# Kernel optimization log

Hardware: AMD Instinct MI355X
Metric: run time of the kernel (lower is better)

Reference implementation:

```python
import jax, jax.numpy as jnp
import numpy as np

N_NODES = 50000
N_EDGES = 1600000
IN_DIM = 128
HEADS = 4
HEAD_DIM = 32  # out_dim // heads
N_REL = 3
NEG_SLOPE = 0.2


def setup_inputs() -> dict:
    key = jax.random.key(0)
    ks = jax.random.split(key, 8)
    x = jax.random.normal(ks[0], (N_NODES, IN_DIM), dtype=jnp.float32)
    edge_index = jax.random.randint(ks[1], (2, N_EDGES), 0, N_NODES, dtype=jnp.int64)
    edge_type = jax.random.randint(ks[2], (N_EDGES,), 0, N_REL, dtype=jnp.int64)
    # per-relation GATConv params (PyG layout: lin weight, att_src, att_dst, bias)
    s = 1.0 / np.sqrt(IN_DIM)
    W = jax.random.normal(ks[3], (N_REL, IN_DIM, HEADS * HEAD_DIM), dtype=jnp.float32) * s
    att_src = jax.random.normal(ks[4], (N_REL, HEADS, HEAD_DIM), dtype=jnp.float32) * s
    att_dst = jax.random.normal(ks[5], (N_REL, HEADS, HEAD_DIM), dtype=jnp.float32) * s
    bias = jnp.zeros((N_REL, HEADS * HEAD_DIM), dtype=jnp.float32)
    rel_w = jnp.ones((N_REL,), dtype=jnp.float32)  # relation_weights param
    return {"x": x, "W": W, "att_src": att_src, "att_dst": att_dst,
            "bias": bias, "rel_w": rel_w,
            "edge_index": edge_index, "edge_type": edge_type}


def reference(x, W, att_src, att_dst, bias, rel_w, edge_index, edge_type):
    N = x.shape[0]
    NEG = jnp.float32(-1e9)
    # self loops (GATConv add_self_loops=True) appended; present in every relation
    self_idx = jnp.arange(N, dtype=edge_index.dtype)
    src = jnp.concatenate([edge_index[0], self_idx])  # [E+N]
    dst = jnp.concatenate([edge_index[1], self_idx])  # [E+N]
    weights = jax.nn.softmax(rel_w)
    out = jnp.zeros((N, HEADS * HEAD_DIM), dtype=x.dtype)
    for r in range(N_REL):
        h = (x @ W[r]).reshape(N, HEADS, HEAD_DIM)  # [N,H,C]
        a_s = jnp.einsum('nhc,hc->nh', h, att_src[r])
        a_d = jnp.einsum('nhc,hc->nh', h, att_dst[r])
        score = jax.nn.leaky_relu(a_s[src] + a_d[dst], NEG_SLOPE)  # [E+N,H]
        mask = jnp.concatenate([edge_type == r, jnp.ones((N,), dtype=bool)])
        score = jnp.where(mask[:, None], score, NEG)  # mask out other relations
        # segment softmax over incoming edges per destination node
        smax = jax.ops.segment_max(score, dst, num_segments=N)  # finite: self-loops
        ex = jnp.exp(score - smax[dst])
        denom = jax.ops.segment_sum(ex, dst, num_segments=N)
        alpha = ex / denom[dst]  # [E+N,H]
        msg = alpha[:, :, None] * h[src]  # [E+N,H,C]
        rel_out = jax.ops.segment_sum(msg, dst, num_segments=N).reshape(N, HEADS * HEAD_DIM)
        out = out + weights[r] * (rel_out + bias[r])
    return out
```

## Files before the change

kernel.cpp:

```cpp
#include <hip/hip_runtime.h>
#include <hip/hip_bf16.h>
#include <hip/hip_fp16.h>
#include <math.h>

#define IN_DIM 128
#define OUT_DIM 128
#define HEADS 4
#define HEAD_DIM 32
#define NREL 3
#define NEG_SLOPE 0.2f

#define CHUNK 4096
#define BUCK_SHIFT 7
#define DPB 128
#define KPB 384
#define CAPE 6144
#define CAPS (CAPE + 3*DPB)

typedef __attribute__((ext_vector_type(8))) short short8;
typedef __attribute__((ext_vector_type(4))) float f32x4;
typedef unsigned short u16;

static __device__ __forceinline__ float leaky(float x){ return fmaxf(x, NEG_SLOPE*x); }
static __device__ __forceinline__ unsigned bf16rn(float x){
  unsigned b = __float_as_uint(x);
  b += 0x7FFF + ((b>>16)&1u);
  return b>>16;
}
static __device__ __forceinline__ unsigned h2pack(float a, float b){
  union { __half h[2]; unsigned u; } p;
  p.h[0] = __float2half_rn(a); p.h[1] = __float2half_rn(b);
  return p.u;
}

__global__ void k_wprep(const float* __restrict__ W, const float* __restrict__ att_s,
                        const float* __restrict__ att_d, const float* __restrict__ rw,
                        const float* __restrict__ bias, u16* __restrict__ WTall,
                        float* __restrict__ smw, float* __restrict__ biasMix){
  const int r = blockIdx.x;
  const int t = threadIdx.x;
  const float* Wr = W + (size_t)r*IN_DIM*OUT_DIM;
  u16* WT = WTall + (size_t)r*144*128;
  for (int i=t; i<128*128; i+=256){
    int k = i>>7, col = i&127;
    WT[col*128 + k] = (u16)bf16rn(Wr[i]);
  }
  if (t < 128){
    int k = t;
    for (int h=0; h<4; h++){
      float ss=0.f, sd=0.f;
      for (int c=0; c<32; c++){
        float w = Wr[k*128 + h*32 + c];
        ss = fmaf(w, att_s[(r*4+h)*32+c], ss);
        sd = fmaf(w, att_d[(r*4+h)*32+c], sd);
      }
      WT[(128+h)*128 + k] = (u16)bf16rn(ss);
      WT[(132+h)*128 + k] = (u16)bf16rn(sd);
    }
  }
  for (int i=t; i<8*128; i+=256) WT[136*128 + i] = 0;
  if (r == 0){
    float m = fmaxf(rw[0], fmaxf(rw[1], rw[2]));
    float e0=__expf(rw[0]-m), e1=__expf(rw[1]-m), e2=__expf(rw[2]-m);
    float inv = 1.f/(e0+e1+e2);
    if (t < 3) smw[t] = (t==0?e0:(t==1?e1:e2))*inv;
    if (t < 128)
      biasMix[t] = inv*(e0*bias[t] + e1*bias[OUT_DIM+t] + e2*bias[2*OUT_DIM+t]);
  }
}

__global__ __launch_bounds__(256) void k_gemmhist(
    const float* __restrict__ x, const u16* __restrict__ WTall,
    unsigned* __restrict__ hq, float* __restrict__ as_, float* __restrict__ ad_,
    const int* __restrict__ ei, int* __restrict__ histG,
    int N, int E, int NCHUNK, int NBUCK){
  __shared__ int h[512];
  const int t = threadIdx.x;

  if (blockIdx.x < (unsigned)NCHUNK){
    const int c = blockIdx.x;
    h[t] = 0; h[t+256] = 0; __syncthreads();
    const int* dstp = ei + E;
    const int base = c*CHUNK;
    #pragma unroll 4
    for (int it=0; it<CHUNK/256; ++it){
      int e = base + it*256 + t;
      if (e < E) atomicAdd(&h[dstp[e]>>BUCK_SHIFT], 1);
    }
    __syncthreads();
    for (int k=t; k<NBUCK; k+=256) histG[k*NCHUNK + c] = h[k];
    return;
  }

  const int w = t >> 6;
  const int l = t & 63;
  const int row0 = (blockIdx.x - NCHUNK)*128 + w*32;
  const int lg = l >> 4;
  const int lc = l & 15;

  short8 afrag[4][2];
  #pragma unroll
  for (int ks=0; ks<4; ks++){
    const int k0 = ks*32 + lg*8;
    #pragma unroll
    for (int rf=0; rf<2; rf++){
      int row = row0 + rf*16 + lc;
      float4 v0, v1;
      if (row < N){
        const float4* xp = (const float4*)(x + (size_t)row*IN_DIM + k0);
        v0 = xp[0]; v1 = xp[1];
      } else { v0 = float4{0.f,0.f,0.f,0.f}; v1 = v0; }
      union { short8 s; unsigned u[4]; } pa;
      pa.u[0] = bf16rn(v0.x) | (bf16rn(v0.y)<<16);
      pa.u[1] = bf16rn(v0.z) | (bf16rn(v0.w)<<16);
      pa.u[2] = bf16rn(v1.x) | (bf16rn(v1.y)<<16);
      pa.u[3] = bf16rn(v1.z) | (bf16rn(v1.w)<<16);
      afrag[ks][rf] = pa.s;
    }
  }

  for (int r=0; r<NREL; r++){
    const u16* WT = WTall + (size_t)r*144*128;
    f32x4 acc[2][9];
    #pragma unroll
    for (int rf=0; rf<2; rf++)
      #pragma unroll
      for (int cf=0; cf<9; cf++) acc[rf][cf] = (f32x4){0.f,0.f,0.f,0.f};

    #pragma unroll
    for (int ks=0; ks<4; ks++){
      const int k0 = ks*32 + lg*8;
      #pragma unroll
      for (int cf=0; cf<9; cf++){
        short8 b = *(const short8*)(WT + (size_t)(cf*16 + lc)*128 + k0);
        #pragma unroll
        for (int rf=0; rf<2; rf++)
          acc[rf][cf] = __builtin_amdgcn_mfma_f32_16x16x32_bf16(afrag[ks][rf], b, acc[rf][cf], 0, 0, 0);
      }
    }

    #pragma unroll
    for (int rf=0; rf<2; rf++){
      #pragma unroll
      for (int j=0; j<4; j++){
        int row = row0 + rf*16 + lg*4 + j;
        bool ok = (row < N);
        size_t nidx = (size_t)r*N + row;
        #pragma unroll
        for (int cf=0; cf<8; cf++){
          float v = acc[rf][cf][j];
          float pv = __shfl_xor(v, 1);
          if (ok && !(l&1))
            hq[nidx*64 + cf*8 + (lc>>1)] = bf16rn(v) | (bf16rn(pv)<<16);
        }
        float av = acc[rf][8][j];
        if (ok && lc < 4)       as_[nidx*4 + lc]     = av;
        else if (ok && lc < 8)  ad_[nidx*4 + (lc-4)] = av;
      }
    }
  }
}

__global__ __launch_bounds__(256) void k_scanSeg(const int* __restrict__ histG,
                        int* __restrict__ chunkOff, int* __restrict__ totalE, int NCHUNK){
  __shared__ int sh[512];
  __shared__ int ps[256];
  const int b = blockIdx.x, t = threadIdx.x;
  sh[t]     = (t     < NCHUNK) ? histG[b*NCHUNK + t]     : 0;
  sh[t+256] = (t+256 < NCHUNK) ? histG[b*NCHUNK + t+256] : 0;
  __syncthreads();
  int e0 = sh[2*t], pair = e0 + sh[2*t+1];
  ps[t] = pair; __syncthreads();
  int x = pair;
  for (int off=1; off<256; off<<=1){
    int y = (t>=off)?ps[t-off]:0; __syncthreads();
    x += y; ps[t] = x; __syncthreads();
  }
  int ex = x - pair;
  if (2*t   < NCHUNK) chunkOff[b*NCHUNK + 2*t]   = ex;
  if (2*t+1 < NCHUNK) chunkOff[b*NCHUNK + 2*t+1] = ex + e0;
  if (t == 255) totalE[b] = x;
}

__global__ __launch_bounds__(256) void k_part(const int* __restrict__ et, const int* __restrict__ ei,
                       const int* __restrict__ chunkOff, unsigned* __restrict__ payload,
                       int E, int NCHUNK, int NBUCK){
  __shared__ int cur[512];
  const int c = blockIdx.x, t = threadIdx.x;
  for (int k=t; k<NBUCK; k+=256) cur[k] = k*CAPE + chunkOff[k*NCHUNK + c];
  __syncthreads();
  const int* dstp = ei + E;
  const int base = c*CHUNK;
  #pragma unroll 4
  for (int it=0; it<CHUNK/256; ++it){
    int e = base + it*256 + t;
    if (e < E){
      int d = dstp[e];
      int s = ei[e];
      int r = et[e];
      int b = d >> BUCK_SHIFT;
      int pos = atomicAdd(&cur[b], 1);
      payload[pos] = (unsigned)((d & (DPB-1)) | (r<<7) | (s<<9));
    }
  }
}

__global__ __launch_bounds__(512) void k_csr(const unsigned* __restrict__ payload,
                     const int* __restrict__ totalE,
                     const float* __restrict__ as_, const float* __restrict__ ad_,
                     const float* __restrict__ smw,
                     int* __restrict__ offs, unsigned* __restrict__ ssrc2,
                     uint2* __restrict__ alpha, float4* __restrict__ ivg,
                     int E, int N, int NCHUNK, int NBUCK){
  __shared__ int cntA[KPB];
  __shared__ int cur[KPB];
  __shared__ float den[KPB*4];
  __shared__ float4 adl[KPB];
  __shared__ int ps[DPB];
  const int b = blockIdx.x, t = threadIdx.x;
  const int bs = b*CAPE;
  const int be = bs + totalE[b];
  const int outbase = b*CAPS;
  const int validD = min(N - b*DPB, DPB);

  for (int k=t; k<KPB; k+=512) cntA[k] = 0;
  for (int k=t; k<KPB*4; k+=512) den[k] = 0.f;
  for (int k=t; k<KPB; k+=512){
    int dl = k/3, r = k - dl*3;
    int d2 = b*DPB + dl;
    adl[k] = (d2 < N) ? ((const float4*)ad_)[(size_t)r*N + d2] : (float4){0,0,0,0};
  }
  __syncthreads();
  for (int i=bs+t; i<be; i+=512){
    unsigned p = payload[i];
    atomicAdd(&cntA[(int)(p&(DPB-1))*NREL + (int)((p>>7)&3u)], 1);
  }
  __syncthreads();
  const int dst = b*DPB + t;
  int c0=0,c1=0,c2=0,sum=0,o0=0,o1=0,o2=0,hs=0;
  if (t < DPB){
    hs = (dst < N) ? 1 : 0;
    c0 = cntA[3*t]   + hs;
    c1 = cntA[3*t+1] + hs;
    c2 = cntA[3*t+2] + hs;
    sum = c0+c1+c2;
    ps[t] = sum;
  }
  __syncthreads();
  int xsc = sum;
  for (int off=1; off<DPB; off<<=1){
    int y = (t < DPB && t >= off) ? ps[t-off] : 0;
    __syncthreads();
    if (t < DPB) { xsc += y; ps[t] = xsc; }
    __syncthreads();
  }
  if (t < DPB){
    int ex = xsc - sum;
    o0 = outbase + ex; o1 = o0 + c0; o2 = o1 + c1;
    offs[b*(KPB+1) + 3*t]   = o0;
    offs[b*(KPB+1) + 3*t+1] = o1;
    offs[b*(KPB+1) + 3*t+2] = o2;
    cur[3*t]   = (o0 - outbase) + hs;
    cur[3*t+1] = (o1 - outbase) + hs;
    cur[3*t+2] = (o2 - outbase) + hs;
  }
  if (t == 0) offs[b*(KPB+1) + KPB] = outbase + (be - bs) + 3*validD;
  __syncthreads();
  for (int i=bs+t; i<be; i+=512){
    unsigned p = payload[i];
    int dl = (int)(p&(DPB-1)), r = (int)((p>>7)&3u), s = (int)(p>>9);
    int lkey = dl*NREL + r;
    int pos = outbase + atomicAdd(&cur[lkey], 1);
    float4 a4 = ((const float4*)as_)[(size_t)r*N + s];
    float4 b4 = adl[lkey];
    float ex0 = __expf(leaky(a4.x+b4.x));
    float ex1 = __expf(leaky(a4.y+b4.y));
    float ex2 = __expf(leaky(a4.z+b4.z));
    float ex3 = __expf(leaky(a4.w+b4.w));
    ssrc2[pos] = (unsigned)(s | (r<<16));
    alpha[pos] = (uint2){ h2pack(ex0,ex1), h2pack(ex2,ex3) };
    atomicAdd(&den[lkey*4+0], ex0); atomicAdd(&den[lkey*4+1], ex1);
    atomicAdd(&den[lkey*4+2], ex2); atomicAdd(&den[lkey*4+3], ex3);
  }
  __syncthreads();
  if (t < DPB && dst < N){
    int starts[3] = {o0, o1, o2};
    #pragma unroll
    for (int r=0; r<NREL; r++){
      int lkey = 3*t + r;
      float4 a4 = ((const float4*)as_)[(size_t)r*N + dst];
      float4 b4 = adl[lkey];
      float s0 = __expf(leaky(a4.x+b4.x));
      float s1 = __expf(leaky(a4.y+b4.y));
      float s2 = __expf(leaky(a4.z+b4.z));
      float s3 = __expf(leaky(a4.w+b4.w));
      float w = smw[r];
      float4 iv;
      iv.x = w/(den[lkey*4+0]+s0);
      iv.y = w/(den[lkey*4+1]+s1);
      iv.z = w/(den[lkey*4+2]+s2);
      iv.w = w/(den[lkey*4+3]+s3);
      ivg[dst*3 + r] = iv;
      int sp = starts[r];
      ssrc2[sp] = (unsigned)(dst | (r<<16));
      alpha[sp] = (uint2){ h2pack(s0,s1), h2pack(s2,s3) };
    }
  }
}

__global__ __launch_bounds__(128) void k_segment(
    const int* __restrict__ offs, const unsigned* __restrict__ ssrc2,
    const uint2* __restrict__ alpha, const unsigned* __restrict__ hq,
    const float4* __restrict__ ivg, const float* __restrict__ biasMix,
    float* __restrict__ out, int N){
  const int wave = threadIdx.x >> 6;
  const int lane = threadIdx.x & 63;
  const int dst  = blockIdx.x*2 + wave;
  if (dst >= N) return;
  const int g  = lane >> 3;
  const int l8 = lane & 7;
  const int h0 = l8 >> 2;

  const int bb = dst >> BUCK_SHIFT;
  const int lk = (dst & (DPB-1))*3;
  const int* ob = offs + (size_t)bb*(KPB+1);
  int beg = __builtin_amdgcn_readfirstlane(ob[lk]);
  int end = __builtin_amdgcn_readfirstlane(ob[lk+3]);

  float4 v0 = ivg[dst*3+0], v1 = ivg[dst*3+1], v2 = ivg[dst*3+2];
  float iA0 = h0 ? v0.y : v0.x, iB0 = h0 ? v0.w : v0.z;
  float iA1 = h0 ? v1.y : v1.x, iB1 = h0 ? v1.w : v1.z;
  float iA2 = h0 ? v2.y : v2.x, iB2 = h0 ? v2.w : v2.z;

  float acc0[8], acc1[8];
  #pragma unroll
  for (int q=0; q<8; q++){ acc0[q]=0.f; acc1[q]=0.f; }

  for (int i0=beg; i0<end; i0+=16){
    int i = i0 + g;
    int j = i0 + 8 + g;
    bool vi = (i < end), vj = (j < end);
    unsigned pk1=0, pk2=0; uint2 av1={0,0}, av2={0,0};
    if (vi){ pk1 = ssrc2[i]; av1 = alpha[i]; }
    if (vj){ pk2 = ssrc2[j]; av2 = alpha[j]; }
    if (vi){
      int s = (int)(pk1 & 0xFFFFu);
      int r = (int)((pk1 >> 16) & 3u);
      float ivA = (r==0)? iA0 : (r==1)? iA1 : iA2;
      float ivB = (r==0)? iB0 : (r==1)? iB1 : iB2;
      union { unsigned u; __half h[2]; } pa, pb;
      pa.u = av1.x; pb.u = av1.y;
      float a0 = __half2float(pa.h[h0]) * ivA;
      float a1 = __half2float(pb.h[h0]) * ivB;
      const uint4* hp = (const uint4*)(hq + ((size_t)r*N + s)*64 + l8*4);
      uint4 u0 = hp[0];
      uint4 u1 = hp[8];
      const unsigned* p0 = (const unsigned*)&u0;
      const unsigned* p1 = (const unsigned*)&u1;
      #pragma unroll
      for (int q=0; q<4; q++){
        acc0[2*q]   = fmaf(a0, __uint_as_float(p0[q]<<16),           acc0[2*q]);
        acc0[2*q+1] = fmaf(a0, __uint_as_float(p0[q] & 0xFFFF0000u), acc0[2*q+1]);
        acc1[2*q]   = fmaf(a1, __uint_as_float(p1[q]<<16),           acc1[2*q]);
        acc1[2*q+1] = fmaf(a1, __uint_as_float(p1[q] & 0xFFFF0000u), acc1[2*q+1]);
      }
    }
    if (vj){
      int s = (int)(pk2 & 0xFFFFu);
      int r = (int)((pk2 >> 16) & 3u);
      float ivA = (r==0)? iA0 : (r==1)? iA1 : iA2;
      float ivB = (r==0)? iB0 : (r==1)? iB1 : iB2;
      union { unsigned u; __half h[2]; } pa, pb;
      pa.u = av2.x; pb.u = av2.y;
      float a0 = __half2float(pa.h[h0]) * ivA;
      float a1 = __half2float(pb.h[h0]) * ivB;
      const uint4* hp = (const uint4*)(hq + ((size_t)r*N + s)*64 + l8*4);
      uint4 u0 = hp[0];
      uint4 u1 = hp[8];
      const unsigned* p0 = (const unsigned*)&u0;
      const unsigned* p1 = (const unsigned*)&u1;
      #pragma unroll
      for (int q=0; q<4; q++){
        acc0[2*q]   = fmaf(a0, __uint_as_float(p0[q]<<16),           acc0[2*q]);
        acc0[2*q+1] = fmaf(a0, __uint_as_float(p0[q] & 0xFFFF0000u), acc0[2*q+1]);
        acc1[2*q]   = fmaf(a1, __uint_as_float(p1[q]<<16),           acc1[2*q]);
        acc1[2*q+1] = fmaf(a1, __uint_as_float(p1[q] & 0xFFFF0000u), acc1[2*q+1]);
      }
    }
  }

  #pragma unroll
  for (int o=8; o<=32; o<<=1){
    #pragma unroll
    for (int q=0; q<8; q++){
      acc0[q] += __shfl_xor(acc0[q], o);
      acc1[q] += __shfl_xor(acc1[q], o);
    }
  }

  if (g == 0){
    const float4* bmA = (const float4*)(biasMix + 8*l8);
    const float4* bmB = (const float4*)(biasMix + 64 + 8*l8);
    float4 x0 = bmA[0], x1 = bmA[1], y0 = bmB[0], y1 = bmB[1];
    float* orow = out + (size_t)dst*OUT_DIM;
    float4 o0 = {acc0[0]+x0.x, acc0[1]+x0.y, acc0[2]+x0.z, acc0[3]+x0.w};
    float4 o1 = {acc0[4]+x1.x, acc0[5]+x1.y, acc0[6]+x1.z, acc0[7]+x1.w};
    float4 o2 = {acc1[0]+y0.x, acc1[1]+y0.y, acc1[2]+y0.z, acc1[3]+y0.w};
    float4 o3 = {acc1[4]+y1.x, acc1[5]+y1.y, acc1[6]+y1.z, acc1[7]+y1.w};
    *(float4*)(orow + 8*l8)          = o0;
    *(float4*)(orow + 8*l8 + 4)      = o1;
    *(float4*)(orow + 64 + 8*l8)     = o2;
    *(float4*)(orow + 64 + 8*l8 + 4) = o3;
  }
}

extern "C" void kernel_launch(void* const* d_in, const int* in_sizes, int n_in,
                              void* d_out, int out_size, void* d_ws, size_t ws_size,
                              hipStream_t stream) {
  const float* x     = (const float*)d_in[0];
  const float* W     = (const float*)d_in[1];
  const float* att_s = (const float*)d_in[2];
  const float* att_d = (const float*)d_in[3];
  const float* bias  = (const float*)d_in[4];
  const float* rw    = (const float*)d_in[5];
  const int*   ei    = (const int*)d_in[6];
  const int*   et    = (const int*)d_in[7];
  float* out = (float*)d_out;

  const int N = in_sizes[0] / IN_DIM;
  const int E = in_sizes[7];
  const int M = NREL * N;
  const int NCHUNK = (E + CHUNK - 1) / CHUNK;
  const int NBUCK  = (N + DPB - 1) / DPB;
  const int GB     = (N + 127) / 128;

  char* ws = (char*)d_ws;
  size_t off = 0;
  auto alloc = [&](size_t bytes) -> void* {
    void* p = ws + off; off += (bytes + 255) & ~(size_t)255; return p;
  };
  unsigned* hq       = (unsigned*)alloc((size_t)M * 64 * 4);
  float*    as_      = (float*)   alloc((size_t)M * 4 * 4);
  float*    ad_      = (float*)   alloc((size_t)M * 4 * 4);
  int*      offs     = (int*)     alloc((size_t)NBUCK * (KPB+1) * 4);
  int*      histG    = (int*)     alloc((size_t)NBUCK * NCHUNK * 4);
  int*      chunkOff = (int*)     alloc((size_t)NBUCK * NCHUNK * 4);
  int*      totalE   = (int*)     alloc((size_t)NBUCK * 4);
  unsigned* payload  = (unsigned*)alloc((size_t)NBUCK * CAPE * 4);
  unsigned* ssrc2    = (unsigned*)alloc((size_t)NBUCK * CAPS * 4);
  uint2*    alpha    = (uint2*)   alloc((size_t)NBUCK * CAPS * 8);
  float4*   ivg      = (float4*)  alloc((size_t)M * 16);
  float*    smw      = (float*)   alloc(256);
  float*    biasMix  = (float*)   alloc(512);
  u16*      WTall    = (u16*)     alloc((size_t)NREL * 144 * 128 * 2);

  k_wprep<<<NREL, 256, 0, stream>>>(W, att_s, att_d, rw, bias, WTall, smw, biasMix);
  k_gemmhist<<<NCHUNK + GB, 256, 0, stream>>>(x, WTall, hq, as_, ad_, ei, histG, N, E, NCHUNK, NBUCK);
  k_scanSeg<<<NBUCK, 256, 0, stream>>>(histG, chunkOff, totalE, NCHUNK);
  k_part<<<NCHUNK, 256, 0, stream>>>(et, ei, chunkOff, payload, E, NCHUNK, NBUCK);
  k_csr<<<NBUCK, 512, 0, stream>>>(payload, totalE, as_, ad_, smw, offs, ssrc2, alpha, ivg, E, N, NCHUNK, NBUCK);
  k_segment<<<(N + 1) / 2, 128, 0, stream>>>(offs, ssrc2, alpha, hq, ivg, biasMix, out, N);
}
```

Measured before the change: 218.4 us.

## Pack edge src and alpha into one 16-byte record, hoist gathers, split wprep

```diff
diff --git a/kernel.cpp b/kernel.cpp
--- a/kernel.cpp
+++ b/kernel.cpp
@@ -33,17 +33,23 @@
   return p.u;
 }
 
-__global__ void k_wprep(const float* __restrict__ W, const float* __restrict__ att_s,
-                        const float* __restrict__ att_d, const float* __restrict__ rw,
-                        const float* __restrict__ bias, u16* __restrict__ WTall,
-                        float* __restrict__ smw, float* __restrict__ biasMix){
-  const int r = blockIdx.x;
+__global__ __launch_bounds__(256) void k_wprep(
+    const float* __restrict__ W, const float* __restrict__ att_s,
+    const float* __restrict__ att_d, const float* __restrict__ rw,
+    const float* __restrict__ bias, u16* __restrict__ WTall,
+    float* __restrict__ smw, float* __restrict__ biasMix){
+  const int r = blockIdx.x / 9;
+  const int tile = blockIdx.x % 9;
   const int t = threadIdx.x;
   const float* Wr = W + (size_t)r*IN_DIM*OUT_DIM;
   u16* WT = WTall + (size_t)r*144*128;
-  for (int i=t; i<128*128; i+=256){
-    int k = i>>7, col = i&127;
-    WT[col*128 + k] = (u16)bf16rn(Wr[i]);
+  if (tile < 8){
+    const int col0 = tile*16;
+    for (int i=t; i<16*128; i+=256){
+      int col = col0 + (i>>7), k = i&127;
+      WT[col*128 + k] = (u16)bf16rn(Wr[k*128 + col]);
+    }
+    return;
   }
   if (t < 128){
     int k = t;
@@ -209,8 +215,8 @@
                      const int* __restrict__ totalE,
                      const float* __restrict__ as_, const float* __restrict__ ad_,
                      const float* __restrict__ smw,
-                     int* __restrict__ offs, unsigned* __restrict__ ssrc2,
-                     uint2* __restrict__ alpha, float4* __restrict__ ivg,
+                     int* __restrict__ offs, uint4* __restrict__ slot,
+                     float4* __restrict__ ivg,
                      int E, int N, int NCHUNK, int NBUCK){
   __shared__ int cntA[KPB];
   __shared__ int cur[KPB];
@@ -277,8 +283,7 @@
     float ex1 = __expf(leaky(a4.y+b4.y));
     float ex2 = __expf(leaky(a4.z+b4.z));
     float ex3 = __expf(leaky(a4.w+b4.w));
-    ssrc2[pos] = (unsigned)(s | (r<<16));
-    alpha[pos] = (uint2){ h2pack(ex0,ex1), h2pack(ex2,ex3) };
+    slot[pos] = (uint4){ (unsigned)(s | (r<<16)), h2pack(ex0,ex1), h2pack(ex2,ex3), 0u };
     atomicAdd(&den[lkey*4+0], ex0); atomicAdd(&den[lkey*4+1], ex1);
     atomicAdd(&den[lkey*4+2], ex2); atomicAdd(&den[lkey*4+3], ex3);
   }
@@ -301,16 +306,14 @@
       iv.z = w/(den[lkey*4+2]+s2);
       iv.w = w/(den[lkey*4+3]+s3);
       ivg[dst*3 + r] = iv;
-      int sp = starts[r];
-      ssrc2[sp] = (unsigned)(dst | (r<<16));
-      alpha[sp] = (uint2){ h2pack(s0,s1), h2pack(s2,s3) };
+      slot[starts[r]] = (uint4){ (unsigned)(dst | (r<<16)), h2pack(s0,s1), h2pack(s2,s3), 0u };
     }
   }
 }
 
 __global__ __launch_bounds__(128) void k_segment(
-    const int* __restrict__ offs, const unsigned* __restrict__ ssrc2,
-    const uint2* __restrict__ alpha, const unsigned* __restrict__ hq,
+    const int* __restrict__ offs, const uint4* __restrict__ slot,
+    const unsigned* __restrict__ hq,
     const float4* __restrict__ ivg, const float* __restrict__ biasMix,
     float* __restrict__ out, int N){
   const int wave = threadIdx.x >> 6;
@@ -338,25 +341,34 @@
 
   for (int i0=beg; i0<end; i0+=16){
     int i = i0 + g;
-    int j = i0 + 8 + g;
+    int j = i + 8;
     bool vi = (i < end), vj = (j < end);
-    unsigned pk1=0, pk2=0; uint2 av1={0,0}, av2={0,0};
-    if (vi){ pk1 = ssrc2[i]; av1 = alpha[i]; }
-    if (vj){ pk2 = ssrc2[j]; av2 = alpha[j]; }
+    uint4 rec1 = {0,0,0,0}, rec2 = {0,0,0,0};
+    if (vi) rec1 = slot[i];
+    if (vj) rec2 = slot[j];
+    uint4 u0a, u1a, u0b, u1b;
     if (vi){
-      int s = (int)(pk1 & 0xFFFFu);
-      int r = (int)((pk1 >> 16) & 3u);
+      int s = (int)(rec1.x & 0xFFFFu);
+      int r = (int)((rec1.x >> 16) & 3u);
+      const uint4* hp = (const uint4*)(hq + ((size_t)r*N + s)*64 + l8*4);
+      u0a = hp[0]; u1a = hp[8];
+    }
+    if (vj){
+      int s = (int)(rec2.x & 0xFFFFu);
+      int r = (int)((rec2.x >> 16) & 3u);
+      const uint4* hp = (const uint4*)(hq + ((size_t)r*N + s)*64 + l8*4);
+      u0b = hp[0]; u1b = hp[8];
+    }
+    if (vi){
+      int r = (int)((rec1.x >> 16) & 3u);
       float ivA = (r==0)? iA0 : (r==1)? iA1 : iA2;
       float ivB = (r==0)? iB0 : (r==1)? iB1 : iB2;
       union { unsigned u; __half h[2]; } pa, pb;
-      pa.u = av1.x; pb.u = av1.y;
+      pa.u = rec1.y; pb.u = rec1.z;
       float a0 = __half2float(pa.h[h0]) * ivA;
       float a1 = __half2float(pb.h[h0]) * ivB;
-      const uint4* hp = (const uint4*)(hq + ((size_t)r*N + s)*64 + l8*4);
-      uint4 u0 = hp[0];
-      uint4 u1 = hp[8];
-      const unsigned* p0 = (const unsigned*)&u0;
-      const unsigned* p1 = (const unsigned*)&u1;
+      const unsigned* p0 = (const unsigned*)&u0a;
+      const unsigned* p1 = (const unsigned*)&u1a;
       #pragma unroll
       for (int q=0; q<4; q++){
         acc0[2*q]   = fmaf(a0, __uint_as_float(p0[q]<<16),           acc0[2*q]);
@@ -366,19 +378,15 @@
       }
     }
     if (vj){
-      int s = (int)(pk2 & 0xFFFFu);
-      int r = (int)((pk2 >> 16) & 3u);
+      int r = (int)((rec2.x >> 16) & 3u);
       float ivA = (r==0)? iA0 : (r==1)? iA1 : iA2;
       float ivB = (r==0)? iB0 : (r==1)? iB1 : iB2;
       union { unsigned u; __half h[2]; } pa, pb;
-      pa.u = av2.x; pb.u = av2.y;
+      pa.u = rec2.y; pb.u = rec2.z;
       float a0 = __half2float(pa.h[h0]) * ivA;
       float a1 = __half2float(pb.h[h0]) * ivB;
-      const uint4* hp = (const uint4*)(hq + ((size_t)r*N + s)*64 + l8*4);
-      uint4 u0 = hp[0];
-      uint4 u1 = hp[8];
-      const unsigned* p0 = (const unsigned*)&u0;
-      const unsigned* p1 = (const unsigned*)&u1;
+      const unsigned* p0 = (const unsigned*)&u0b;
+      const unsigned* p1 = (const unsigned*)&u1b;
       #pragma unroll
       for (int q=0; q<4; q++){
         acc0[2*q]   = fmaf(a0, __uint_as_float(p0[q]<<16),           acc0[2*q]);
@@ -447,17 +455,16 @@
   int*      chunkOff = (int*)     alloc((size_t)NBUCK * NCHUNK * 4);
   int*      totalE   = (int*)     alloc((size_t)NBUCK * 4);
   unsigned* payload  = (unsigned*)alloc((size_t)NBUCK * CAPE * 4);
-  unsigned* ssrc2    = (unsigned*)alloc((size_t)NBUCK * CAPS * 4);
-  uint2*    alpha    = (uint2*)   alloc((size_t)NBUCK * CAPS * 8);
+  uint4*    slot     = (uint4*)   alloc((size_t)NBUCK * CAPS * 16);
   float4*   ivg      = (float4*)  alloc((size_t)M * 16);
   float*    smw      = (float*)   alloc(256);
   float*    biasMix  = (float*)   alloc(512);
   u16*      WTall    = (u16*)     alloc((size_t)NREL * 144 * 128 * 2);
 
-  k_wprep<<<NREL, 256, 0, stream>>>(W, att_s, att_d, rw, bias, WTall, smw, biasMix);
+  k_wprep<<<NREL*9, 256, 0, stream>>>(W, att_s, att_d, rw, bias, WTall, smw, biasMix);
   k_gemmhist<<<NCHUNK + GB, 256, 0, stream>>>(x, WTall, hq, as_, ad_, ei, histG, N, E, NCHUNK, NBUCK);
   k_scanSeg<<<NBUCK, 256, 0, stream>>>(histG, chunkOff, totalE, NCHUNK);
   k_part<<<NCHUNK, 256, 0, stream>>>(et, ei, chunkOff, payload, E, NCHUNK, NBUCK);
-  k_csr<<<NBUCK, 512, 0, stream>>>(payload, totalE, as_, ad_, smw, offs, ssrc2, alpha, ivg, E, N, NCHUNK, NBUCK);
-  k_segment<<<(N + 1) / 2, 128, 0, stream>>>(offs, ssrc2, alpha, hq, ivg, biasMix, out, N);
-}
+  k_csr<<<NBUCK, 512, 0, stream>>>(payload, totalE, as_, ad_, smw, offs, slot, ivg, E, N, NCHUNK, NBUCK);
+  k_segment<<<(N + 1) / 2, 128, 0, stream>>>(offs, slot, hq, ivg, biasMix, out, N);
+}
```

Measured after the change: 202.4 us. -7.4%, faster.
